# Kernel tuning notes

Measured on AMD Instinct MI355X. Metric: run time of the kernel, lower is better.

The kernel has to match this reference:

```python
import jax, jax.numpy as jnp
import numpy as np

D = 32          # d_lat // 2
D_ANCIL = 16
HID = 128
GRID = 64
N = GRID * GRID # n_patch / n_state
B = 8
DT = 0.25
T_MAX = 4.0
N_STEPS = 18    # enough half/full Strang steps to exceed T_MAX for all batch elems


def _grid_neighbours(g):
    # 4 nearest neighbours on a periodic g x g dual mesh
    idx = np.arange(g * g).reshape(g, g)
    nbrs = np.stack([np.roll(idx, 1, 0), np.roll(idx, -1, 0),
                     np.roll(idx, 1, 1), np.roll(idx, -1, 1)], axis=-1)
    return jnp.asarray(nbrs.reshape(g * g, 4), dtype=jnp.int32)


def setup_inputs() -> dict:
    key = jax.random.key(0)
    ks = jax.random.split(key, 8)
    din = 2 * D + D_ANCIL  # concat(z, neighbour-mean z, xi)
    s1 = 1.0 / np.sqrt(din)
    s2 = 1.0 / np.sqrt(HID)
    return {
        "x": jax.random.normal(ks[0], (B, N, 2 * D + D_ANCIL), jnp.float32),
        "t_final": jax.random.uniform(ks[1], (B,), jnp.float32) * T_MAX,
        "W1_q": jax.random.normal(ks[2], (din, HID), jnp.float32) * s1,
        "b1_q": jnp.zeros((HID,), jnp.float32),
        "W2_q": jax.random.normal(ks[3], (HID, D), jnp.float32) * s2,
        "b2_q": jnp.zeros((D,), jnp.float32),
        "W1_p": jax.random.normal(ks[4], (din, HID), jnp.float32) * s1,
        "b1_p": jnp.zeros((HID,), jnp.float32),
        "W2_p": jax.random.normal(ks[5], (HID, D), jnp.float32) * s2,
        "b2_p": jnp.zeros((D,), jnp.float32),
        "nbrs": _grid_neighbours(GRID),
    }


def _F(z, xi, nbrs, W1, b1, W2, b2):
    # nearest-neighbour forcing: per-node MLP on (z, mean of neighbour z, xi)
    z_nbr = jnp.mean(z[:, nbrs, :], axis=2)           # (B,N,4,D) -> (B,N,D)
    h = jnp.tanh(jnp.concatenate([z, z_nbr, xi], axis=-1) @ W1 + b1)
    return h @ W2 + b2                                 # (B,N,D)


def _masked_stepsize(t, t_final, dt):
    # per-batch stepsize, clipped so integration stops exactly at t_final
    return jnp.clip(t_final - t, 0.0, dt)


def reference(x, t_final, W1_q, b1_q, W2_q, b2_q, W1_p, b1_p, W2_p, b2_p, nbrs):
    q = x[..., :D]
    p = x[..., D:2 * D]
    xi = x[..., 2 * D:]
    tf = t_final[:, None, None]  # broadcast over (N, D)

    def step(carry, k):
        q, p, t_q, t_p = carry
        rho = jnp.where(k == 0, jnp.float32(0.5), jnp.float32(1.0))
        dt_q = _masked_stepsize(t_q, tf, rho * DT)
        q = q + dt_q * _F(p, xi, nbrs, W1_q, b1_q, W2_q, b2_q)
        t_q = t_q + rho * DT
        dt_p = _masked_stepsize(t_p, tf, DT)
        p = p + dt_p * _F(q, xi, nbrs, W1_p, b1_p, W2_p, b2_p)
        t_p = t_p + DT
        return (q, p, t_q, t_p), None

    init = (q, p, jnp.float32(0.0), jnp.float32(0.0))
    (q, p, _, _), _ = jax.lax.scan(step, init, jnp.arange(N_STEPS))
    return jnp.concatenate([q, p, xi], axis=-1)
```

## Files before the change

kernel.cpp:

```cpp
#include <hip/hip_runtime.h>
#include <hip/hip_bf16.h>

#define GRID_W 64
#define NPTS   4096
#define BATCH  8
#define DD     32
#define DIN    80
#define HID    128
#define SH_STRIDE 136
#define SQ_STRIDE 36
#define NBLK   512
#define NSTEP  34
#define SPIN_CAP 8192
#define OFF_F1Q 131072
#define OFF_F2Q (OFF_F1Q + 24*64*16)
#define OFF_F1P (OFF_F2Q + 8*64*16)
#define OFF_F2P (OFF_F1P + 24*64*16)
#define OFF_EBUF 262144
#define EB_U64_TOTAL ((size_t)NBLK * 64 * 24)
#define WS_NEED ((size_t)OFF_EBUF + EB_U64_TOTAL * 8)

typedef __attribute__((ext_vector_type(8))) short short8;
typedef __attribute__((ext_vector_type(4))) float f32x4;
typedef unsigned long long u64;

__device__ __forceinline__ ushort f2bf(float v) {
    __hip_bfloat16 h = __float2bfloat16(v);
    return __builtin_bit_cast(ushort, h);
}
__device__ __forceinline__ uint packbf(float a, float b) {
    return (uint)f2bf(a) | ((uint)f2bf(b) << 16);
}
__device__ __forceinline__ short8 pack8(float4 a, float4 b) {
    union { uint u[4]; short8 s; } t;
    t.u[0] = packbf(a.x, a.y); t.u[1] = packbf(a.z, a.w);
    t.u[2] = packbf(b.x, b.y); t.u[3] = packbf(b.z, b.w);
    return t.s;
}
__device__ __forceinline__ float bf2f(ushort u) {
    union { uint i; float f; } t; t.i = ((uint)u) << 16; return t.f;
}

__device__ __forceinline__ u64 ld_sys64(const u64* p) {
    return __hip_atomic_load(p, __ATOMIC_RELAXED, __HIP_MEMORY_SCOPE_SYSTEM);
}
__device__ __forceinline__ void st_sys64(u64* p, u64 v) {
    __hip_atomic_store(p, v, __ATOMIC_RELAXED, __HIP_MEMORY_SCOPE_SYSTEM);
}

__global__ void setup_all(const float* __restrict__ x, float* __restrict__ out,
                          char* __restrict__ ws,
                          const float* __restrict__ W1q, const float* __restrict__ W2q,
                          const float* __restrict__ W1p, const float* __restrict__ W2p,
                          int do_ebuf)
{
    const int blk = blockIdx.x, tid = threadIdx.x;
    if (blk >= NBLK) {
        const int s = blk - NBLK;
        const float* W1 = s ? W1p : W1q;
        const float* W2 = s ? W2p : W2q;
        ushort* f1 = (ushort*)(ws + (s ? OFF_F1P : OFF_F1Q));
        ushort* f2 = (ushort*)(ws + (s ? OFF_F2P : OFF_F2Q));
        for (int idx = tid; idx < 24 * 512; idx += 256) {
            int f = idx >> 9, rem = idx & 511, lane = rem >> 3, j = rem & 7;
            int ks = f >> 3, nt = f & 7;
            int k = ks * 32 + (lane >> 4) * 8 + j, n = nt * 16 + (lane & 15);
            f1[idx] = f2bf(k < DIN ? W1[k * HID + n] : 0.0f);
        }
        for (int idx = tid; idx < 8 * 512; idx += 256) {
            int f = idx >> 9, rem = idx & 511, lane = rem >> 3, j = rem & 7;
            int ks = f >> 1, nt = f & 1;
            int k = ks * 32 + (lane >> 4) * 8 + j, n = nt * 16 + (lane & 15);
            f2[idx] = f2bf(W2[k * DD + n]);
        }
        return;
    }
    const int b = blk >> 6, r = blk & 63;
    const int pt = tid >> 2, j4 = tid & 3;
    const float* src = x + (size_t)(b * NPTS + r * GRID_W + pt) * DIN;
    {
        float* dst = out + (size_t)(b * NPTS + r * GRID_W + pt) * DIN + j4 * 20;
        const float* s4 = src + j4 * 20;
        #pragma unroll
        for (int i = 0; i < 5; ++i)
            *(float4*)(dst + i * 4) = *(const float4*)(s4 + i * 4);
    }
    if (do_ebuf) {
        u64* drow = (u64*)(ws + OFF_EBUF) + ((size_t)((b * 64 + r) * 64) + pt) * 24;
        #pragma unroll
        for (int k = 0; k < 6; ++k) {
            const int m = j4 * 6 + k;
            const int half = m / 12, sub = m % 12;
            const int qR = sub / 3, u = sub - qR * 3;
            const int sbase = qR * 8 + u * 3, cap = qR * 8 + 7;
            const int i1 = (sbase + 1 > cap) ? cap : sbase + 1;
            const int i2 = (sbase + 2 > cap) ? cap : sbase + 2;
            const float* hs = src + (half ? DD : 0);
            u64 pk = (u64)f2bf(hs[sbase]) | ((u64)f2bf(hs[i1]) << 16)
                   | ((u64)f2bf(hs[i2]) << 32);
            drow[half * 12 + qR * 3 + u] = pk;
        }
    }
}

struct Acc2 { f32x4 a0, a1; };

__device__ __forceinline__ Acc2 eval_F(short8 af0, short8 af1, short8 af2,
    const short8* __restrict__ F1, const short8* __restrict__ w2,
    const float* __restrict__ B1, ushort* __restrict__ sH,
    int wv, int lane, int l16, int quad, int q8)
{
    f32x4 acc1[8];
    #pragma unroll
    for (int nt = 0; nt < 8; ++nt) acc1[nt] = (f32x4){0.f, 0.f, 0.f, 0.f};
    #pragma unroll
    for (int nt = 0; nt < 8; ++nt)
        acc1[nt] = __builtin_amdgcn_mfma_f32_16x16x32_bf16(af0, F1[nt * 64 + lane], acc1[nt], 0, 0, 0);
    #pragma unroll
    for (int nt = 0; nt < 8; ++nt)
        acc1[nt] = __builtin_amdgcn_mfma_f32_16x16x32_bf16(af1, F1[(8 + nt) * 64 + lane], acc1[nt], 0, 0, 0);
    #pragma unroll
    for (int nt = 0; nt < 8; ++nt)
        acc1[nt] = __builtin_amdgcn_mfma_f32_16x16x32_bf16(af2, F1[(16 + nt) * 64 + lane], acc1[nt], 0, 0, 0);
    #pragma unroll
    for (int nt = 0; nt < 8; ++nt) {
        const int col = nt * 16 + l16;
        const float bias = B1[col];
        #pragma unroll
        for (int rg = 0; rg < 4; ++rg) {
            const int rowm = wv * 16 + quad * 4 + rg;
            float s = acc1[nt][rg] + bias;
            float e = __expf(2.0f * s);
            float hh = 1.0f - __fdividef(2.0f, e + 1.0f);
            sH[rowm * SH_STRIDE + col] = f2bf(hh);
        }
    }
    Acc2 o;
    o.a0 = (f32x4){0.f, 0.f, 0.f, 0.f};
    o.a1 = (f32x4){0.f, 0.f, 0.f, 0.f};
    #pragma unroll
    for (int ks = 0; ks < 4; ++ks) {
        short8 af = *(const short8*)&sH[(wv * 16 + l16) * SH_STRIDE + ks * 32 + q8];
        o.a0 = __builtin_amdgcn_mfma_f32_16x16x32_bf16(af, w2[ks * 2 + 0], o.a0, 0, 0, 0);
        o.a1 = __builtin_amdgcn_mfma_f32_16x16x32_bf16(af, w2[ks * 2 + 1], o.a1, 0, 0, 0);
    }
    return o;
}

__global__ __launch_bounds__(256, 2) void sympl_coop(
    float* __restrict__ out, const float* __restrict__ tfinal,
    char* __restrict__ ws,
    const float* __restrict__ b1q, const float* __restrict__ b2q,
    const float* __restrict__ b1p, const float* __restrict__ b2p)
{
    __shared__ __align__(16) float  sQ[64 * SQ_STRIDE];
    __shared__ __align__(16) float  sP[64 * SQ_STRIDE];
    __shared__ __align__(16) ushort sH[64 * SH_STRIDE];
    __shared__ __align__(16) float  sO[4 * 512];
    __shared__ uint ldsF[4];

    u64* eb = (u64*)(ws + OFF_EBUF);
    const int blk = blockIdx.x, tid = threadIdx.x;
    const int b = blk >> 6, r = blk & 63;
    const int wv = tid >> 6, lane = tid & 63;
    const int l16 = lane & 15, quad = lane >> 4, q8 = quad * 8;
    const int c = wv * 16 + l16;
    const int rm = (r + 63) & 63, rp = (r + 1) & 63;
    const int cm = (c + 63) & 63, cp = (c + 1) & 63;
    const int pt = tid >> 2, sg = (tid & 3) * 8;

    const u64* prm = eb + ((size_t)(b * 64 + rm) * 64 + c) * 24 + quad * 3;
    const u64* prp = eb + ((size_t)(b * 64 + rp) * 64 + c) * 24 + quad * 3;
    const u64* s_rm = eb + ((size_t)(b * 64 + rm) * 64 + (wv * 16 + 15)) * 24 + 11;
    const u64* s_rp = eb + ((size_t)(b * 64 + rp) * 64 + (wv * 16 + 15)) * 24 + 11;
    u64* pub = eb + ((size_t)(b * 64 + r) * 64) * 24;

    {
        const float* src = out + (size_t)(b * NPTS + r * GRID_W + pt) * DIN;
        *(float4*)&sQ[pt * SQ_STRIDE + sg]     = *(const float4*)(src + sg);
        *(float4*)&sQ[pt * SQ_STRIDE + sg + 4] = *(const float4*)(src + sg + 4);
        *(float4*)&sP[pt * SQ_STRIDE + sg]     = *(const float4*)(src + DD + sg);
        *(float4*)&sP[pt * SQ_STRIDE + sg + 4] = *(const float4*)(src + DD + sg + 4);
    }
    if (tid < 4) ldsF[tid] = 0;
    short8 af2;
    if (quad < 2) {
        const float* px = out + (size_t)(b * NPTS + r * GRID_W + c) * DIN + 2 * DD + q8;
        af2 = pack8(*(const float4*)px, *(const float4*)(px + 4));
    } else {
        af2 = (short8)(short)0;
    }
    short8 w2q[8], w2p[8];
    {
        const short8* F2q = (const short8*)(ws + OFF_F2Q);
        const short8* F2p = (const short8*)(ws + OFF_F2P);
        #pragma unroll
        for (int i = 0; i < 8; ++i) { w2q[i] = F2q[i * 64 + lane]; w2p[i] = F2p[i * 64 + lane]; }
    }
    const float tf = tfinal[b];
    __syncthreads();

    const int wl = (wv + 3) & 3, wr = (wv + 1) & 3;

    float tq = 0.0f, tp = 0.0f;
    #pragma unroll 1
    for (int h = 0; h < NSTEP; ++h) {
        const int phase = h & 1;
        const float dtmax = phase ? 0.25f : ((h == 0) ? 0.125f : 0.25f);
        const float tcur  = phase ? tp : tq;
        if (!phase && tq >= tf) break;
        const float dt = fminf(fmaxf(tf - tcur, 0.0f), dtmax);
        const int srcH = phase ^ 1;
        const int dstH = phase;
        const float* srcL = phase ? sQ : sP;
        float*       dstL = phase ? sP : sQ;
        const short8* F1 = (const short8*)(ws + (phase ? OFF_F1P : OFF_F1Q));
        const uint hh = (uint)h;

        f32x4 acc1[8];
        if (dt > 0.0f) {
            const float* s0p = srcL + c * SQ_STRIDE + q8;
            float4 a0 = *(const float4*)s0p, a1 = *(const float4*)(s0p + 4);
            short8 af0 = pack8(a0, a1);
            #pragma unroll
            for (int nt = 0; nt < 8; ++nt) acc1[nt] = (f32x4){0.f, 0.f, 0.f, 0.f};
            #pragma unroll
            for (int nt = 0; nt < 8; ++nt)
                acc1[nt] = __builtin_amdgcn_mfma_f32_16x16x32_bf16(af0, F1[nt * 64 + lane], acc1[nt], 0, 0, 0);
            #pragma unroll
            for (int nt = 0; nt < 8; ++nt)
                acc1[nt] = __builtin_amdgcn_mfma_f32_16x16x32_bf16(af2, F1[(16 + nt) * 64 + lane], acc1[nt], 0, 0, 0);
        }

        {
            int spins = 0;
            while (true) {
                bool ok = true;
                if (lane == 0)      ok = ((uint)(ld_sys64(s_rm + srcH * 12) >> 48) == hh);
                else if (lane == 1) ok = ((uint)(ld_sys64(s_rp + srcH * 12) >> 48) == hh);
                else if (lane == 2) ok = (__hip_atomic_load(&ldsF[wl], __ATOMIC_RELAXED, __HIP_MEMORY_SCOPE_WORKGROUP) >= hh);
                else if (lane == 3) ok = (__hip_atomic_load(&ldsF[wr], __ATOMIC_RELAXED, __HIP_MEMORY_SCOPE_WORKGROUP) >= hh);
                if (__all((int)ok)) break;
                if (++spins > SPIN_CAP) break;
                __builtin_amdgcn_s_sleep(1);
            }
        }

        if (dt > 0.0f) {
            const u64* pA = prm + srcH * 12;
            const u64* pB = prp + srcH * 12;
            u64 a0, a1, a2, c0, c1, c2;
            int spins = 0;
            while (true) {
                a0 = ld_sys64(pA);     a1 = ld_sys64(pA + 1); a2 = ld_sys64(pA + 2);
                c0 = ld_sys64(pB);     c1 = ld_sys64(pB + 1); c2 = ld_sys64(pB + 2);
                bool ok = ((uint)(a0 >> 48) == hh) & ((uint)(a1 >> 48) == hh)
                        & ((uint)(a2 >> 48) == hh) & ((uint)(c0 >> 48) == hh)
                        & ((uint)(c1 >> 48) == hh) & ((uint)(c2 >> 48) == hh);
                if (__all((int)ok)) break;
                if (++spins > SPIN_CAP) break;
                __builtin_amdgcn_s_sleep(1);
            }

            const float* smp = srcL + cm * SQ_STRIDE + q8;
            const float* spp = srcL + cp * SQ_STRIDE + q8;
            float4 lf0 = *(const float4*)smp, lf1 = *(const float4*)(smp + 4);
            float4 rt0 = *(const float4*)spp, rt1 = *(const float4*)(spp + 4);
            float4 m0, m1;
            m0.x = 0.25f * (bf2f((ushort)a0)         + bf2f((ushort)c0)         + lf0.x + rt0.x);
            m0.y = 0.25f * (bf2f((ushort)(a0 >> 16)) + bf2f((ushort)(c0 >> 16)) + lf0.y + rt0.y);
            m0.z = 0.25f * (bf2f((ushort)(a0 >> 32)) + bf2f((ushort)(c0 >> 32)) + lf0.z + rt0.z);
            m0.w = 0.25f * (bf2f((ushort)a1)         + bf2f((ushort)c1)         + lf0.w + rt0.w);
            m1.x = 0.25f * (bf2f((ushort)(a1 >> 16)) + bf2f((ushort)(c1 >> 16)) + lf1.x + rt1.x);
            m1.y = 0.25f * (bf2f((ushort)(a1 >> 32)) + bf2f((ushort)(c1 >> 32)) + lf1.y + rt1.y);
            m1.z = 0.25f * (bf2f((ushort)a2)         + bf2f((ushort)c2)         + lf1.z + rt1.z);
            m1.w = 0.25f * (bf2f((ushort)(a2 >> 16)) + bf2f((ushort)(c2 >> 16)) + lf1.w + rt1.w);
            short8 af1 = pack8(m0, m1);
            #pragma unroll
            for (int nt = 0; nt < 8; ++nt)
                acc1[nt] = __builtin_amdgcn_mfma_f32_16x16x32_bf16(af1, F1[(8 + nt) * 64 + lane], acc1[nt], 0, 0, 0);

            const float* B1 = phase ? b1p : b1q;
            #pragma unroll
            for (int nt = 0; nt < 8; ++nt) {
                const int col = nt * 16 + l16;
                const float bias = B1[col];
                #pragma unroll
                for (int rg = 0; rg < 4; ++rg) {
                    const int rowm = wv * 16 + quad * 4 + rg;
                    float s = acc1[nt][rg] + bias;
                    float e = __expf(2.0f * s);
                    float hhv = 1.0f - __fdividef(2.0f, e + 1.0f);
                    sH[rowm * SH_STRIDE + col] = f2bf(hhv);
                }
            }
            const short8* w2 = phase ? w2p : w2q;
            f32x4 o0 = (f32x4){0.f, 0.f, 0.f, 0.f};
            f32x4 o1 = (f32x4){0.f, 0.f, 0.f, 0.f};
            #pragma unroll
            for (int ks = 0; ks < 4; ++ks) {
                short8 af = *(const short8*)&sH[(wv * 16 + l16) * SH_STRIDE + ks * 32 + q8];
                o0 = __builtin_amdgcn_mfma_f32_16x16x32_bf16(af, w2[ks * 2 + 0], o0, 0, 0, 0);
                o1 = __builtin_amdgcn_mfma_f32_16x16x32_bf16(af, w2[ks * 2 + 1], o1, 0, 0, 0);
            }
            float* sOw = sO + wv * 512;
            const float* B2 = phase ? b2p : b2q;
            #pragma unroll
            for (int nt = 0; nt < 2; ++nt) {
                const int col = nt * 16 + l16;
                const float b2v = B2[col];
                const f32x4 av = nt ? o1 : o0;
                #pragma unroll
                for (int rg = 0; rg < 4; ++rg)
                    sOw[(quad * 4 + rg) * DD + col] = av[rg] + b2v;
            }
            #pragma unroll
            for (int it = 0; it < 2; ++it) {
                const int slot = lane + it * 64;
                const int lr = slot >> 3, seg = (slot & 7) * 4;
                const int pt_ = wv * 16 + lr;
                const float* po = &sOw[lr * DD + seg];
                float* pl = dstL + pt_ * SQ_STRIDE + seg;
                float4 o = *(const float4*)pl;
                o.x += dt * po[0]; o.y += dt * po[1];
                o.z += dt * po[2]; o.w += dt * po[3];
                *(float4*)pl = o;
            }
            const u64 tg = ((u64)(ushort)(hh + 1)) << 48;
            #pragma unroll
            for (int t = 0; t < 3; ++t) {
                const int g = t * 64 + lane;
                const int pt_ = g / 12, sub = g - pt_ * 12;
                const int qR = sub / 3, u = sub - qR * 3;
                const int sbase = qR * 8 + u * 3, cap = qR * 8 + 7;
                const int i1 = (sbase + 1 > cap) ? cap : sbase + 1;
                const int i2 = (sbase + 2 > cap) ? cap : sbase + 2;
                const float* pd = dstL + (wv * 16 + pt_) * SQ_STRIDE;
                u64 pk = (u64)f2bf(pd[sbase]) | ((u64)f2bf(pd[i1]) << 16)
                       | ((u64)f2bf(pd[i2]) << 32) | tg;
                st_sys64(pub + (size_t)(wv * 16 + pt_) * 24 + dstH * 12 + qR * 3 + u, pk);
            }
        }
        __asm__ volatile("s_waitcnt lgkmcnt(0)" ::: "memory");
        if (lane == 0)
            __hip_atomic_store(&ldsF[wv], (uint)(h + 1), __ATOMIC_RELAXED, __HIP_MEMORY_SCOPE_WORKGROUP);
        if (phase) tp += dtmax; else tq += dtmax;
    }

    {
        float* dst = out + (size_t)(b * NPTS + r * GRID_W + pt) * DIN;
        *(float4*)(dst + sg)          = *(const float4*)&sQ[pt * SQ_STRIDE + sg];
        *(float4*)(dst + sg + 4)      = *(const float4*)&sQ[pt * SQ_STRIDE + sg + 4];
        *(float4*)(dst + DD + sg)     = *(const float4*)&sP[pt * SQ_STRIDE + sg];
        *(float4*)(dst + DD + sg + 4) = *(const float4*)&sP[pt * SQ_STRIDE + sg + 4];
    }
}

__global__ __launch_bounds__(256, 2) void sympl_step(
    float* __restrict__ state, const float* __restrict__ tfinal,
    const char* __restrict__ ws,
    const float* __restrict__ B1, const float* __restrict__ B2,
    int phase, float tcur, float dtmax)
{
    __shared__ __align__(16) ushort sH[64 * SH_STRIDE];
    __shared__ __align__(16) float  sO[4 * 512];
    const int blk = blockIdx.x, tid = threadIdx.x;
    const int wv = tid >> 6, lane = tid & 63;
    const int l16 = lane & 15, quad = lane >> 4, q8 = quad * 8;
    const int b = blk >> 6, r = blk & 63;
    const int c = wv * 16 + l16;

    const float tf = tfinal[b];
    const float dt = fminf(fmaxf(tf - tcur, 0.0f), dtmax);
    if (dt <= 0.0f) return;

    const int srcoff = phase ? 0 : DD;
    const int dstoff = phase ? DD : 0;
    float* bb = state + (size_t)b * NPTS * DIN;
    const float* selfp = bb + (r * GRID_W + c) * DIN;
    const int rm = (r + 63) & 63, rp = (r + 1) & 63;
    const int cm = (c + 63) & 63, cp = (c + 1) & 63;
    short8 af0, af1, af2;
    {
        const float* ps = selfp + srcoff + q8;
        af0 = pack8(*(const float4*)ps, *(const float4*)(ps + 4));
    }
    {
        const float* p0 = bb + (rm * GRID_W + c) * DIN + srcoff + q8;
        const float* p1 = bb + (rp * GRID_W + c) * DIN + srcoff + q8;
        const float* p2 = bb + (r * GRID_W + cm) * DIN + srcoff + q8;
        const float* p3 = bb + (r * GRID_W + cp) * DIN + srcoff + q8;
        float4 a0 = *(const float4*)p0, a1 = *(const float4*)(p0 + 4);
        float4 b0 = *(const float4*)p1, b1v = *(const float4*)(p1 + 4);
        float4 c0 = *(const float4*)p2, c1 = *(const float4*)(p2 + 4);
        float4 d0 = *(const float4*)p3, d1 = *(const float4*)(p3 + 4);
        float4 m0, m1;
        m0.x = 0.25f * (a0.x + b0.x + c0.x + d0.x);
        m0.y = 0.25f * (a0.y + b0.y + c0.y + d0.y);
        m0.z = 0.25f * (a0.z + b0.z + c0.z + d0.z);
        m0.w = 0.25f * (a0.w + b0.w + c0.w + d0.w);
        m1.x = 0.25f * (a1.x + b1v.x + c1.x + d1.x);
        m1.y = 0.25f * (a1.y + b1v.y + c1.y + d1.y);
        m1.z = 0.25f * (a1.z + b1v.z + c1.z + d1.z);
        m1.w = 0.25f * (a1.w + b1v.w + c1.w + d1.w);
        af1 = pack8(m0, m1);
    }
    if (quad < 2) {
        const float* px = selfp + 2 * DD + q8;
        af2 = pack8(*(const float4*)px, *(const float4*)(px + 4));
    } else {
        af2 = (short8)(short)0;
    }
    const short8* F1 = (const short8*)(ws + (phase ? OFF_F1P : OFF_F1Q));
    const short8* F2 = (const short8*)(ws + (phase ? OFF_F2P : OFF_F2Q));
    short8 w2[8];
    #pragma unroll
    for (int i = 0; i < 8; ++i) w2[i] = F2[i * 64 + lane];
    Acc2 A = eval_F(af0, af1, af2, F1, w2, B1, sH, wv, lane, l16, quad, q8);
    float* sOw = sO + wv * 512;
    #pragma unroll
    for (int nt = 0; nt < 2; ++nt) {
        const int col = nt * 16 + l16;
        const float b2v = B2[col];
        const f32x4 av = nt ? A.a1 : A.a0;
        #pragma unroll
        for (int rg = 0; rg < 4; ++rg)
            sOw[(quad * 4 + rg) * DD + col] = av[rg] + b2v;
    }
    #pragma unroll
    for (int it = 0; it < 2; ++it) {
        const int slot = lane + it * 64;
        const int lr = slot >> 3, seg = (slot & 7) * 4;
        float* pd = bb + (r * GRID_W + wv * 16 + lr) * DIN + dstoff + seg;
        const float* po = &sOw[lr * DD + seg];
        float4 o = *(const float4*)pd;
        o.x += dt * po[0]; o.y += dt * po[1];
        o.z += dt * po[2]; o.w += dt * po[3];
        *(float4*)pd = o;
    }
}

extern "C" void kernel_launch(void* const* d_in, const int* in_sizes, int n_in,
                              void* d_out, int out_size, void* d_ws, size_t ws_size,
                              hipStream_t stream)
{
    const float* x   = (const float*)d_in[0];
    const float* tf  = (const float*)d_in[1];
    const float* W1q = (const float*)d_in[2];
    const float* b1q = (const float*)d_in[3];
    const float* W2q = (const float*)d_in[4];
    const float* b2q = (const float*)d_in[5];
    const float* W1p = (const float*)d_in[6];
    const float* b1p = (const float*)d_in[7];
    const float* W2p = (const float*)d_in[8];
    const float* b2p = (const float*)d_in[9];
    float* out = (float*)d_out;
    char* ws = (char*)d_ws;

    const int coop_ok = (ws_size >= WS_NEED) ? 1 : 0;

    setup_all<<<dim3(NBLK + 2), dim3(256), 0, stream>>>(x, out, ws, W1q, W2q,
                                                        W1p, W2p, coop_ok);

    if (coop_ok) {
        sympl_coop<<<dim3(NBLK), dim3(256), 0, stream>>>(
            out, tf, ws, b1q, b2q, b1p, b2p);
    } else {
        float tq = 0.0f, tp = 0.0f;
        for (int h = 0; h < NSTEP; ++h) {
            const int phase = h & 1;
            const float dtmax = phase ? 0.25f : ((h == 0) ? 0.125f : 0.25f);
            const float tcur  = phase ? tp : tq;
            sympl_step<<<dim3(NBLK), dim3(256), 0, stream>>>(
                out, tf, ws, phase ? b1p : b1q, phase ? b2p : b2q,
                phase, tcur, dtmax);
            if (phase) tp += dtmax; else tq += dtmax;
        }
    }
}
```

Baseline: 222.0 us.

## Replace per-half-step neighbour sync with one per full step via halo recompute

The cooperative kernel now synchronises with neighbouring row blocks once per full Strang step instead of once per half step. Each block recomputes the q update of its two neighbour rows redundantly, using p halos two rows away, so it can run the p half-step without waiting. Exchange buffers are double-buffered by parity, with an initial tag written at setup. Cross-block waits are halved, at the cost of three extra MLP evaluations per step and more LDS.

```diff
diff --git a/kernel.cpp b/kernel.cpp
--- a/kernel.cpp
+++ b/kernel.cpp
@@ -9,16 +9,18 @@
 #define HID    128
 #define SH_STRIDE 136
 #define SQ_STRIDE 36
+#define HB     40
 #define NBLK   512
 #define NSTEP  34
+#define NFULL  17
 #define SPIN_CAP 8192
 #define OFF_F1Q 131072
 #define OFF_F2Q (OFF_F1Q + 24*64*16)
 #define OFF_F1P (OFF_F2Q + 8*64*16)
 #define OFF_F2P (OFF_F1P + 24*64*16)
 #define OFF_EBUF 262144
-#define EB_U64_TOTAL ((size_t)NBLK * 64 * 24)
-#define WS_NEED ((size_t)OFF_EBUF + EB_U64_TOTAL * 8)
+#define EB_PAR ((size_t)NBLK * 64 * 24)
+#define WS_NEED ((size_t)OFF_EBUF + 2 * EB_PAR * 8)
 
 typedef __attribute__((ext_vector_type(8))) short short8;
 typedef __attribute__((ext_vector_type(4))) float f32x4;
@@ -39,6 +41,14 @@
 }
 __device__ __forceinline__ float bf2f(ushort u) {
     union { uint i; float f; } t; t.i = ((uint)u) << 16; return t.f;
+}
+__device__ __forceinline__ short8 u3_to_s8(u64 a, u64 b, u64 c) {
+    union { uint w[4]; short8 s; } t;
+    t.w[0] = (uint)a;
+    t.w[1] = (uint)((a >> 32) & 0xFFFFull) | (((uint)(b & 0xFFFFull)) << 16);
+    t.w[2] = (uint)(b >> 16);
+    t.w[3] = (uint)c;
+    return t.s;
 }
 
 __device__ __forceinline__ u64 ld_sys64(const u64* p) {
@@ -99,6 +109,7 @@
             u64 pk = (u64)f2bf(hs[sbase]) | ((u64)f2bf(hs[i1]) << 16)
                    | ((u64)f2bf(hs[i2]) << 32);
             drow[half * 12 + qR * 3 + u] = pk;
+            drow[EB_PAR + half * 12 + qR * 3 + u] = pk | (0xFFFFull << 48);
         }
     }
 }
@@ -157,7 +168,12 @@
     __shared__ __align__(16) float  sP[64 * SQ_STRIDE];
     __shared__ __align__(16) ushort sH[64 * SH_STRIDE];
     __shared__ __align__(16) float  sO[4 * 512];
-    __shared__ uint ldsF[4];
+    __shared__ __align__(16) ushort hPm[64 * HB];
+    __shared__ __align__(16) ushort hPp[64 * HB];
+    __shared__ __align__(16) ushort hQm[64 * HB];
+    __shared__ __align__(16) ushort hQp[64 * HB];
+    __shared__ __align__(16) ushort hQNm[64 * HB];
+    __shared__ __align__(16) ushort hQNp[64 * HB];
 
     u64* eb = (u64*)(ws + OFF_EBUF);
     const int blk = blockIdx.x, tid = threadIdx.x;
@@ -166,13 +182,16 @@
     const int l16 = lane & 15, quad = lane >> 4, q8 = quad * 8;
     const int c = wv * 16 + l16;
     const int rm = (r + 63) & 63, rp = (r + 1) & 63;
+    const int rm2 = (r + 62) & 63, rp2 = (r + 2) & 63;
     const int cm = (c + 63) & 63, cp = (c + 1) & 63;
     const int pt = tid >> 2, sg = (tid & 3) * 8;
 
-    const u64* prm = eb + ((size_t)(b * 64 + rm) * 64 + c) * 24 + quad * 3;
-    const u64* prp = eb + ((size_t)(b * 64 + rp) * 64 + c) * 24 + quad * 3;
-    const u64* s_rm = eb + ((size_t)(b * 64 + rm) * 64 + (wv * 16 + 15)) * 24 + 11;
-    const u64* s_rp = eb + ((size_t)(b * 64 + rp) * 64 + (wv * 16 + 15)) * 24 + 11;
+    const u64* bq_rm = eb + ((size_t)(b * 64 + rm ) * 64 + c) * 24 + quad * 3;
+    const u64* bq_rp = eb + ((size_t)(b * 64 + rp ) * 64 + c) * 24 + quad * 3;
+    const u64* bp_rm = bq_rm + 12;
+    const u64* bp_rp = bq_rp + 12;
+    const u64* bp_m2 = eb + ((size_t)(b * 64 + rm2) * 64 + c) * 24 + 12 + quad * 3;
+    const u64* bp_p2 = eb + ((size_t)(b * 64 + rp2) * 64 + c) * 24 + 12 + quad * 3;
     u64* pub = eb + ((size_t)(b * 64 + r) * 64) * 24;
 
     {
@@ -182,13 +201,16 @@
         *(float4*)&sP[pt * SQ_STRIDE + sg]     = *(const float4*)(src + DD + sg);
         *(float4*)&sP[pt * SQ_STRIDE + sg + 4] = *(const float4*)(src + DD + sg + 4);
     }
-    if (tid < 4) ldsF[tid] = 0;
-    short8 af2;
+    short8 af2o, af2m, af2p;
     if (quad < 2) {
-        const float* px = out + (size_t)(b * NPTS + r * GRID_W + c) * DIN + 2 * DD + q8;
-        af2 = pack8(*(const float4*)px, *(const float4*)(px + 4));
+        const float* pxo = out + (size_t)(b * NPTS + r  * GRID_W + c) * DIN + 2 * DD + q8;
+        const float* pxm = out + (size_t)(b * NPTS + rm * GRID_W + c) * DIN + 2 * DD + q8;
+        const float* pxp = out + (size_t)(b * NPTS + rp * GRID_W + c) * DIN + 2 * DD + q8;
+        af2o = pack8(*(const float4*)pxo, *(const float4*)(pxo + 4));
+        af2m = pack8(*(const float4*)pxm, *(const float4*)(pxm + 4));
+        af2p = pack8(*(const float4*)pxp, *(const float4*)(pxp + 4));
     } else {
-        af2 = (short8)(short)0;
+        af2o = (short8)(short)0; af2m = (short8)(short)0; af2p = (short8)(short)0;
     }
     short8 w2q[8], w2p[8];
     {
@@ -198,118 +220,75 @@
         for (int i = 0; i < 8; ++i) { w2q[i] = F2q[i * 64 + lane]; w2p[i] = F2p[i * 64 + lane]; }
     }
     const float tf = tfinal[b];
+    const short8* F1q = (const short8*)(ws + OFF_F1Q);
+    const short8* F1p = (const short8*)(ws + OFF_F1P);
+    float* sOw = sO + wv * 512;
     __syncthreads();
-
-    const int wl = (wv + 3) & 3, wr = (wv + 1) & 3;
 
     float tq = 0.0f, tp = 0.0f;
     #pragma unroll 1
-    for (int h = 0; h < NSTEP; ++h) {
-        const int phase = h & 1;
-        const float dtmax = phase ? 0.25f : ((h == 0) ? 0.125f : 0.25f);
-        const float tcur  = phase ? tp : tq;
-        if (!phase && tq >= tf) break;
-        const float dt = fminf(fmaxf(tf - tcur, 0.0f), dtmax);
-        const int srcH = phase ^ 1;
-        const int dstH = phase;
-        const float* srcL = phase ? sQ : sP;
-        float*       dstL = phase ? sP : sQ;
-        const short8* F1 = (const short8*)(ws + (phase ? OFF_F1P : OFF_F1Q));
-        const uint hh = (uint)h;
-
-        f32x4 acc1[8];
-        if (dt > 0.0f) {
-            const float* s0p = srcL + c * SQ_STRIDE + q8;
-            float4 a0 = *(const float4*)s0p, a1 = *(const float4*)(s0p + 4);
-            short8 af0 = pack8(a0, a1);
-            #pragma unroll
-            for (int nt = 0; nt < 8; ++nt) acc1[nt] = (f32x4){0.f, 0.f, 0.f, 0.f};
-            #pragma unroll
-            for (int nt = 0; nt < 8; ++nt)
-                acc1[nt] = __builtin_amdgcn_mfma_f32_16x16x32_bf16(af0, F1[nt * 64 + lane], acc1[nt], 0, 0, 0);
-            #pragma unroll
-            for (int nt = 0; nt < 8; ++nt)
-                acc1[nt] = __builtin_amdgcn_mfma_f32_16x16x32_bf16(af2, F1[(16 + nt) * 64 + lane], acc1[nt], 0, 0, 0);
-        }
-
+    for (int k = 0; k < NFULL; ++k) {
+        if (tq >= tf) break;
+        const float dtq = fminf(tf - tq, (k == 0) ? 0.125f : 0.25f);
+        const float dtp = fminf(fmaxf(tf - tp, 0.0f), 0.25f);
+        const uint kk = (uint)k;
+        const size_t par_r = (size_t)(k & 1) * EB_PAR;
+        const size_t par_w = (size_t)((k + 1) & 1) * EB_PAR;
+
+        u64 vqm0, vqm1, vqm2, vqp0, vqp1, vqp2;
+        u64 vpm0, vpm1, vpm2, vpp0, vpp1, vpp2;
+        u64 vm20, vm21, vm22, vp20, vp21, vp22;
         {
             int spins = 0;
             while (true) {
-                bool ok = true;
-                if (lane == 0)      ok = ((uint)(ld_sys64(s_rm + srcH * 12) >> 48) == hh);
-                else if (lane == 1) ok = ((uint)(ld_sys64(s_rp + srcH * 12) >> 48) == hh);
-                else if (lane == 2) ok = (__hip_atomic_load(&ldsF[wl], __ATOMIC_RELAXED, __HIP_MEMORY_SCOPE_WORKGROUP) >= hh);
-                else if (lane == 3) ok = (__hip_atomic_load(&ldsF[wr], __ATOMIC_RELAXED, __HIP_MEMORY_SCOPE_WORKGROUP) >= hh);
-                if (__all((int)ok)) break;
+                vqm0 = ld_sys64(bq_rm + par_r);     vqm1 = ld_sys64(bq_rm + par_r + 1); vqm2 = ld_sys64(bq_rm + par_r + 2);
+                vqp0 = ld_sys64(bq_rp + par_r);     vqp1 = ld_sys64(bq_rp + par_r + 1); vqp2 = ld_sys64(bq_rp + par_r + 2);
+                vpm0 = ld_sys64(bp_rm + par_r);     vpm1 = ld_sys64(bp_rm + par_r + 1); vpm2 = ld_sys64(bp_rm + par_r + 2);
+                vpp0 = ld_sys64(bp_rp + par_r);     vpp1 = ld_sys64(bp_rp + par_r + 1); vpp2 = ld_sys64(bp_rp + par_r + 2);
+                vm20 = ld_sys64(bp_m2 + par_r);     vm21 = ld_sys64(bp_m2 + par_r + 1); vm22 = ld_sys64(bp_m2 + par_r + 2);
+                vp20 = ld_sys64(bp_p2 + par_r);     vp21 = ld_sys64(bp_p2 + par_r + 1); vp22 = ld_sys64(bp_p2 + par_r + 2);
+                uint bad = 0;
+                bad |= (uint)(vqm0 >> 48) ^ kk; bad |= (uint)(vqm1 >> 48) ^ kk; bad |= (uint)(vqm2 >> 48) ^ kk;
+                bad |= (uint)(vqp0 >> 48) ^ kk; bad |= (uint)(vqp1 >> 48) ^ kk; bad |= (uint)(vqp2 >> 48) ^ kk;
+                bad |= (uint)(vpm0 >> 48) ^ kk; bad |= (uint)(vpm1 >> 48) ^ kk; bad |= (uint)(vpm2 >> 48) ^ kk;
+                bad |= (uint)(vpp0 >> 48) ^ kk; bad |= (uint)(vpp1 >> 48) ^ kk; bad |= (uint)(vpp2 >> 48) ^ kk;
+                bad |= (uint)(vm20 >> 48) ^ kk; bad |= (uint)(vm21 >> 48) ^ kk; bad |= (uint)(vm22 >> 48) ^ kk;
+                bad |= (uint)(vp20 >> 48) ^ kk; bad |= (uint)(vp21 >> 48) ^ kk; bad |= (uint)(vp22 >> 48) ^ kk;
+                if (__all((int)(bad == 0))) break;
                 if (++spins > SPIN_CAP) break;
                 __builtin_amdgcn_s_sleep(1);
             }
         }
-
-        if (dt > 0.0f) {
-            const u64* pA = prm + srcH * 12;
-            const u64* pB = prp + srcH * 12;
-            u64 a0, a1, a2, c0, c1, c2;
-            int spins = 0;
-            while (true) {
-                a0 = ld_sys64(pA);     a1 = ld_sys64(pA + 1); a2 = ld_sys64(pA + 2);
-                c0 = ld_sys64(pB);     c1 = ld_sys64(pB + 1); c2 = ld_sys64(pB + 2);
-                bool ok = ((uint)(a0 >> 48) == hh) & ((uint)(a1 >> 48) == hh)
-                        & ((uint)(a2 >> 48) == hh) & ((uint)(c0 >> 48) == hh)
-                        & ((uint)(c1 >> 48) == hh) & ((uint)(c2 >> 48) == hh);
-                if (__all((int)ok)) break;
-                if (++spins > SPIN_CAP) break;
-                __builtin_amdgcn_s_sleep(1);
-            }
-
-            const float* smp = srcL + cm * SQ_STRIDE + q8;
-            const float* spp = srcL + cp * SQ_STRIDE + q8;
-            float4 lf0 = *(const float4*)smp, lf1 = *(const float4*)(smp + 4);
-            float4 rt0 = *(const float4*)spp, rt1 = *(const float4*)(spp + 4);
-            float4 m0, m1;
-            m0.x = 0.25f * (bf2f((ushort)a0)         + bf2f((ushort)c0)         + lf0.x + rt0.x);
-            m0.y = 0.25f * (bf2f((ushort)(a0 >> 16)) + bf2f((ushort)(c0 >> 16)) + lf0.y + rt0.y);
-            m0.z = 0.25f * (bf2f((ushort)(a0 >> 32)) + bf2f((ushort)(c0 >> 32)) + lf0.z + rt0.z);
-            m0.w = 0.25f * (bf2f((ushort)a1)         + bf2f((ushort)c1)         + lf0.w + rt0.w);
-            m1.x = 0.25f * (bf2f((ushort)(a1 >> 16)) + bf2f((ushort)(c1 >> 16)) + lf1.x + rt1.x);
-            m1.y = 0.25f * (bf2f((ushort)(a1 >> 32)) + bf2f((ushort)(c1 >> 32)) + lf1.y + rt1.y);
-            m1.z = 0.25f * (bf2f((ushort)a2)         + bf2f((ushort)c2)         + lf1.z + rt1.z);
-            m1.w = 0.25f * (bf2f((ushort)(a2 >> 16)) + bf2f((ushort)(c2 >> 16)) + lf1.w + rt1.w);
-            short8 af1 = pack8(m0, m1);
-            #pragma unroll
-            for (int nt = 0; nt < 8; ++nt)
-                acc1[nt] = __builtin_amdgcn_mfma_f32_16x16x32_bf16(af1, F1[(8 + nt) * 64 + lane], acc1[nt], 0, 0, 0);
-
-            const float* B1 = phase ? b1p : b1q;
-            #pragma unroll
-            for (int nt = 0; nt < 8; ++nt) {
-                const int col = nt * 16 + l16;
-                const float bias = B1[col];
-                #pragma unroll
-                for (int rg = 0; rg < 4; ++rg) {
-                    const int rowm = wv * 16 + quad * 4 + rg;
-                    float s = acc1[nt][rg] + bias;
-                    float e = __expf(2.0f * s);
-                    float hhv = 1.0f - __fdividef(2.0f, e + 1.0f);
-                    sH[rowm * SH_STRIDE + col] = f2bf(hhv);
-                }
-            }
-            const short8* w2 = phase ? w2p : w2q;
-            f32x4 o0 = (f32x4){0.f, 0.f, 0.f, 0.f};
-            f32x4 o1 = (f32x4){0.f, 0.f, 0.f, 0.f};
-            #pragma unroll
-            for (int ks = 0; ks < 4; ++ks) {
-                short8 af = *(const short8*)&sH[(wv * 16 + l16) * SH_STRIDE + ks * 32 + q8];
-                o0 = __builtin_amdgcn_mfma_f32_16x16x32_bf16(af, w2[ks * 2 + 0], o0, 0, 0, 0);
-                o1 = __builtin_amdgcn_mfma_f32_16x16x32_bf16(af, w2[ks * 2 + 1], o1, 0, 0, 0);
-            }
-            float* sOw = sO + wv * 512;
-            const float* B2 = phase ? b2p : b2q;
+        *(short8*)&hQm[c * HB + q8] = u3_to_s8(vqm0, vqm1, vqm2);
+        *(short8*)&hQp[c * HB + q8] = u3_to_s8(vqp0, vqp1, vqp2);
+        *(short8*)&hPm[c * HB + q8] = u3_to_s8(vpm0, vpm1, vpm2);
+        *(short8*)&hPp[c * HB + q8] = u3_to_s8(vpp0, vpp1, vpp2);
+        const short8 prm2 = u3_to_s8(vm20, vm21, vm22);
+        const short8 prp2 = u3_to_s8(vp20, vp21, vp22);
+        __syncthreads();
+
+        float pself[8];
+        {
+            const float* sc = &sP[c * SQ_STRIDE + q8];
+            float4 s0 = *(const float4*)sc, s1 = *(const float4*)(sc + 4);
+            pself[0] = s0.x; pself[1] = s0.y; pself[2] = s0.z; pself[3] = s0.w;
+            pself[4] = s1.x; pself[5] = s1.y; pself[6] = s1.z; pself[7] = s1.w;
+        }
+        {
+            short8 af0 = *(const short8*)&hPm[c * HB + q8];
+            short8 ecm = *(const short8*)&hPm[cm * HB + q8];
+            short8 ecp = *(const short8*)&hPm[cp * HB + q8];
+            union { ushort u[8]; short8 s; } m;
+            #pragma unroll
+            for (int j = 0; j < 8; ++j)
+                m.u[j] = f2bf(0.25f * (bf2f((ushort)ecm[j]) + bf2f((ushort)ecp[j])
+                                     + pself[j] + bf2f((ushort)prm2[j])));
+            Acc2 A = eval_F(af0, m.s, af2m, F1q, w2q, b1q, sH, wv, lane, l16, quad, q8);
             #pragma unroll
             for (int nt = 0; nt < 2; ++nt) {
                 const int col = nt * 16 + l16;
-                const float b2v = B2[col];
-                const f32x4 av = nt ? o1 : o0;
+                const float b2v = b2q[col];
+                const f32x4 av = nt ? A.a1 : A.a0;
                 #pragma unroll
                 for (int rg = 0; rg < 4; ++rg)
                     sOw[(quad * 4 + rg) * DD + col] = av[rg] + b2v;
@@ -320,13 +299,87 @@
                 const int lr = slot >> 3, seg = (slot & 7) * 4;
                 const int pt_ = wv * 16 + lr;
                 const float* po = &sOw[lr * DD + seg];
-                float* pl = dstL + pt_ * SQ_STRIDE + seg;
+                u64 old4 = *(const u64*)&hQm[pt_ * HB + seg];
+                float o0 = bf2f((ushort)old4)         + dtq * po[0];
+                float o1 = bf2f((ushort)(old4 >> 16)) + dtq * po[1];
+                float o2 = bf2f((ushort)(old4 >> 32)) + dtq * po[2];
+                float o3 = bf2f((ushort)(old4 >> 48)) + dtq * po[3];
+                *(u64*)&hQNm[pt_ * HB + seg] =
+                    (u64)f2bf(o0) | ((u64)f2bf(o1) << 16) | ((u64)f2bf(o2) << 32) | ((u64)f2bf(o3) << 48);
+            }
+        }
+        {
+            short8 af0 = *(const short8*)&hPp[c * HB + q8];
+            short8 ecm = *(const short8*)&hPp[cm * HB + q8];
+            short8 ecp = *(const short8*)&hPp[cp * HB + q8];
+            union { ushort u[8]; short8 s; } m;
+            #pragma unroll
+            for (int j = 0; j < 8; ++j)
+                m.u[j] = f2bf(0.25f * (bf2f((ushort)ecm[j]) + bf2f((ushort)ecp[j])
+                                     + pself[j] + bf2f((ushort)prp2[j])));
+            Acc2 A = eval_F(af0, m.s, af2p, F1q, w2q, b1q, sH, wv, lane, l16, quad, q8);
+            #pragma unroll
+            for (int nt = 0; nt < 2; ++nt) {
+                const int col = nt * 16 + l16;
+                const float b2v = b2q[col];
+                const f32x4 av = nt ? A.a1 : A.a0;
+                #pragma unroll
+                for (int rg = 0; rg < 4; ++rg)
+                    sOw[(quad * 4 + rg) * DD + col] = av[rg] + b2v;
+            }
+            #pragma unroll
+            for (int it = 0; it < 2; ++it) {
+                const int slot = lane + it * 64;
+                const int lr = slot >> 3, seg = (slot & 7) * 4;
+                const int pt_ = wv * 16 + lr;
+                const float* po = &sOw[lr * DD + seg];
+                u64 old4 = *(const u64*)&hQp[pt_ * HB + seg];
+                float o0 = bf2f((ushort)old4)         + dtq * po[0];
+                float o1 = bf2f((ushort)(old4 >> 16)) + dtq * po[1];
+                float o2 = bf2f((ushort)(old4 >> 32)) + dtq * po[2];
+                float o3 = bf2f((ushort)(old4 >> 48)) + dtq * po[3];
+                *(u64*)&hQNp[pt_ * HB + seg] =
+                    (u64)f2bf(o0) | ((u64)f2bf(o1) << 16) | ((u64)f2bf(o2) << 32) | ((u64)f2bf(o3) << 48);
+            }
+        }
+        {
+            const float* s0p = &sP[c * SQ_STRIDE + q8];
+            short8 af0 = pack8(*(const float4*)s0p, *(const float4*)(s0p + 4));
+            short8 hm = *(const short8*)&hPm[c * HB + q8];
+            short8 hp = *(const short8*)&hPp[c * HB + q8];
+            const float* smp = &sP[cm * SQ_STRIDE + q8];
+            const float* spp = &sP[cp * SQ_STRIDE + q8];
+            float4 l0 = *(const float4*)smp, l1 = *(const float4*)(smp + 4);
+            float4 r0 = *(const float4*)spp, r1 = *(const float4*)(spp + 4);
+            float lv[8] = { l0.x, l0.y, l0.z, l0.w, l1.x, l1.y, l1.z, l1.w };
+            float rv[8] = { r0.x, r0.y, r0.z, r0.w, r1.x, r1.y, r1.z, r1.w };
+            union { ushort u[8]; short8 s; } m;
+            #pragma unroll
+            for (int j = 0; j < 8; ++j)
+                m.u[j] = f2bf(0.25f * (bf2f((ushort)hm[j]) + bf2f((ushort)hp[j]) + lv[j] + rv[j]));
+            Acc2 A = eval_F(af0, m.s, af2o, F1q, w2q, b1q, sH, wv, lane, l16, quad, q8);
+            #pragma unroll
+            for (int nt = 0; nt < 2; ++nt) {
+                const int col = nt * 16 + l16;
+                const float b2v = b2q[col];
+                const f32x4 av = nt ? A.a1 : A.a0;
+                #pragma unroll
+                for (int rg = 0; rg < 4; ++rg)
+                    sOw[(quad * 4 + rg) * DD + col] = av[rg] + b2v;
+            }
+            #pragma unroll
+            for (int it = 0; it < 2; ++it) {
+                const int slot = lane + it * 64;
+                const int lr = slot >> 3, seg = (slot & 7) * 4;
+                const int pt_ = wv * 16 + lr;
+                const float* po = &sOw[lr * DD + seg];
+                float* pl = sQ + pt_ * SQ_STRIDE + seg;
                 float4 o = *(const float4*)pl;
-                o.x += dt * po[0]; o.y += dt * po[1];
-                o.z += dt * po[2]; o.w += dt * po[3];
+                o.x += dtq * po[0]; o.y += dtq * po[1];
+                o.z += dtq * po[2]; o.w += dtq * po[3];
                 *(float4*)pl = o;
             }
-            const u64 tg = ((u64)(ushort)(hh + 1)) << 48;
+            const u64 tg = ((u64)(ushort)(kk + 1)) << 48;
             #pragma unroll
             for (int t = 0; t < 3; ++t) {
                 const int g = t * 64 + lane;
@@ -335,16 +388,68 @@
                 const int sbase = qR * 8 + u * 3, cap = qR * 8 + 7;
                 const int i1 = (sbase + 1 > cap) ? cap : sbase + 1;
                 const int i2 = (sbase + 2 > cap) ? cap : sbase + 2;
-                const float* pd = dstL + (wv * 16 + pt_) * SQ_STRIDE;
+                const float* pd = sQ + (wv * 16 + pt_) * SQ_STRIDE;
                 u64 pk = (u64)f2bf(pd[sbase]) | ((u64)f2bf(pd[i1]) << 16)
                        | ((u64)f2bf(pd[i2]) << 32) | tg;
-                st_sys64(pub + (size_t)(wv * 16 + pt_) * 24 + dstH * 12 + qR * 3 + u, pk);
-            }
-        }
-        __asm__ volatile("s_waitcnt lgkmcnt(0)" ::: "memory");
-        if (lane == 0)
-            __hip_atomic_store(&ldsF[wv], (uint)(h + 1), __ATOMIC_RELAXED, __HIP_MEMORY_SCOPE_WORKGROUP);
-        if (phase) tp += dtmax; else tq += dtmax;
+                st_sys64(pub + par_w + (size_t)(wv * 16 + pt_) * 24 + 0 * 12 + qR * 3 + u, pk);
+            }
+        }
+        __syncthreads();
+
+        if (dtp > 0.0f) {
+            const float* s0p = &sQ[c * SQ_STRIDE + q8];
+            short8 af0 = pack8(*(const float4*)s0p, *(const float4*)(s0p + 4));
+            short8 hm = *(const short8*)&hQNm[c * HB + q8];
+            short8 hp = *(const short8*)&hQNp[c * HB + q8];
+            const float* smp = &sQ[cm * SQ_STRIDE + q8];
+            const float* spp = &sQ[cp * SQ_STRIDE + q8];
+            float4 l0 = *(const float4*)smp, l1 = *(const float4*)(smp + 4);
+            float4 r0 = *(const float4*)spp, r1 = *(const float4*)(spp + 4);
+            float lv[8] = { l0.x, l0.y, l0.z, l0.w, l1.x, l1.y, l1.z, l1.w };
+            float rv[8] = { r0.x, r0.y, r0.z, r0.w, r1.x, r1.y, r1.z, r1.w };
+            union { ushort u[8]; short8 s; } m;
+            #pragma unroll
+            for (int j = 0; j < 8; ++j)
+                m.u[j] = f2bf(0.25f * (bf2f((ushort)hm[j]) + bf2f((ushort)hp[j]) + lv[j] + rv[j]));
+            Acc2 A = eval_F(af0, m.s, af2o, F1p, w2p, b1p, sH, wv, lane, l16, quad, q8);
+            #pragma unroll
+            for (int nt = 0; nt < 2; ++nt) {
+                const int col = nt * 16 + l16;
+                const float b2v = b2p[col];
+                const f32x4 av = nt ? A.a1 : A.a0;
+                #pragma unroll
+                for (int rg = 0; rg < 4; ++rg)
+                    sOw[(quad * 4 + rg) * DD + col] = av[rg] + b2v;
+            }
+            #pragma unroll
+            for (int it = 0; it < 2; ++it) {
+                const int slot = lane + it * 64;
+                const int lr = slot >> 3, seg = (slot & 7) * 4;
+                const int pt_ = wv * 16 + lr;
+                const float* po = &sOw[lr * DD + seg];
+                float* pl = sP + pt_ * SQ_STRIDE + seg;
+                float4 o = *(const float4*)pl;
+                o.x += dtp * po[0]; o.y += dtp * po[1];
+                o.z += dtp * po[2]; o.w += dtp * po[3];
+                *(float4*)pl = o;
+            }
+            const u64 tg = ((u64)(ushort)(kk + 1)) << 48;
+            #pragma unroll
+            for (int t = 0; t < 3; ++t) {
+                const int g = t * 64 + lane;
+                const int pt_ = g / 12, sub = g - pt_ * 12;
+                const int qR = sub / 3, u = sub - qR * 3;
+                const int sbase = qR * 8 + u * 3, cap = qR * 8 + 7;
+                const int i1 = (sbase + 1 > cap) ? cap : sbase + 1;
+                const int i2 = (sbase + 2 > cap) ? cap : sbase + 2;
+                const float* pd = sP + (wv * 16 + pt_) * SQ_STRIDE;
+                u64 pk = (u64)f2bf(pd[sbase]) | ((u64)f2bf(pd[i1]) << 16)
+                       | ((u64)f2bf(pd[i2]) << 32) | tg;
+                st_sys64(pub + par_w + (size_t)(wv * 16 + pt_) * 24 + 1 * 12 + qR * 3 + u, pk);
+            }
+        }
+        tq += (k == 0) ? 0.125f : 0.25f;
+        tp += 0.25f;
     }
 
     {
```

Result: slower. 493.7 us (+122.3%).
